# Kernel optimization log

Measured on AMD Instinct MI355X. Metric: run time of the kernel, lower is better.

## Reference

```python
import jax, jax.numpy as jnp
import numpy as np
import math

N_HEADS = 16
DIM = 1024
D_HEAD = DIM // N_HEADS
BS, QLEN = 2, 2048


def setup_inputs() -> dict:
    key = jax.random.key(0)
    ks = jax.random.split(key, 10)
    s = 0.02
    return {
        "input": jax.random.normal(ks[0], (BS, QLEN, DIM), dtype=jnp.float32),
        "mask": jnp.ones((BS, QLEN), dtype=jnp.int32),
        "q_w": jax.random.normal(ks[1], (DIM, DIM), dtype=jnp.float32) * s,
        "q_b": jax.random.normal(ks[2], (DIM,), dtype=jnp.float32) * s,
        "k_w": jax.random.normal(ks[3], (DIM, DIM), dtype=jnp.float32) * s,
        "k_b": jax.random.normal(ks[4], (DIM,), dtype=jnp.float32) * s,
        "v_w": jax.random.normal(ks[5], (DIM, DIM), dtype=jnp.float32) * s,
        "v_b": jax.random.normal(ks[6], (DIM,), dtype=jnp.float32) * s,
        "o_w": jax.random.normal(ks[7], (DIM, DIM), dtype=jnp.float32) * s,
        "o_b": jax.random.normal(ks[8], (DIM,), dtype=jnp.float32) * s,
    }


def _shape(x, bs):
    # (bs, len, dim) -> (bs, heads, len, d_head)
    return x.reshape(bs, -1, N_HEADS, D_HEAD).transpose(0, 2, 1, 3)


def reference(input, mask, q_w, q_b, k_w, k_b, v_w, v_b, o_w, o_b):
    bs, qlen, dim = input.shape
    # projections (torch Linear: x @ W^T + b)
    q = _shape(input @ q_w.T + q_b, bs)
    k = _shape(input @ k_w.T + k_b, bs)
    v = _shape(input @ v_w.T + v_b, bs)
    q = q / math.sqrt(D_HEAD)
    # scores: (bs, heads, qlen, klen)
    scores = jnp.einsum("bhqd,bhkd->bhqk", q, k)
    pad = (mask == 0)[:, None, None, :]  # (bs,1,1,klen)
    scores = jnp.where(pad, -jnp.inf, scores)
    weights = jax.nn.softmax(scores.astype(jnp.float32), axis=-1).astype(scores.dtype)
    # dropout p=0.0 (eval) -> identity
    context = jnp.einsum("bhqk,bhkd->bhqd", weights, v)
    context = context.transpose(0, 2, 1, 3).reshape(bs, qlen, dim)
    return context @ o_w.T + o_b
```

## Files before the change

kernel.cpp:

```cpp
#include <hip/hip_runtime.h>


#define BS    2
#define QLEN  2048
#define DIM   1024
#define NH    16
#define DH    64
#define MTOK  (BS * QLEN)

#define QSCALE 0.18033688011112042f

typedef __attribute__((ext_vector_type(8))) short short8;
typedef __attribute__((ext_vector_type(4))) float float4_t;
typedef __attribute__((ext_vector_type(4))) int   int4_t;

__device__ __forceinline__ ushort f2bf(float f) {
    unsigned u = __float_as_uint(f);
    return (ushort)((u + 0x7fffu + ((u >> 16) & 1u)) >> 16);
}
__device__ __forceinline__ short8 pack8(float4 a0, float4 a1) {
    short8 r;
    r[0] = (short)f2bf(a0.x); r[1] = (short)f2bf(a0.y);
    r[2] = (short)f2bf(a0.z); r[3] = (short)f2bf(a0.w);
    r[4] = (short)f2bf(a1.x); r[5] = (short)f2bf(a1.y);
    r[6] = (short)f2bf(a1.z); r[7] = (short)f2bf(a1.w);
    return r;
}

__device__ __forceinline__ void glds16(const void* g, void* l) {
    __builtin_amdgcn_global_load_lds(
        (const __attribute__((address_space(1))) unsigned int*)g,
        (__attribute__((address_space(3))) unsigned int*)l, 16, 0, 0);
}

__global__ __launch_bounds__(256) void conv_all(
    const float* __restrict__ x,  const float* __restrict__ qw,
    const float* __restrict__ kw, const float* __restrict__ vw,
    const float* __restrict__ ow,
    ushort* __restrict__ Xbf, ushort* __restrict__ Wbf)
{
    const int blk = blockIdx.x;
    const float* s; ushort* d; size_t base;
    if (blk < 4096)      { s = x;  d = Xbf;             base = (size_t)blk * 1024; }
    else if (blk < 5120) { s = qw; d = Wbf;             base = (size_t)(blk - 4096) * 1024; }
    else if (blk < 6144) { s = kw; d = Wbf + 1048576;   base = (size_t)(blk - 5120) * 1024; }
    else if (blk < 7168) { s = vw; d = Wbf + 2097152;   base = (size_t)(blk - 6144) * 1024; }
    else                 { s = ow; d = Wbf + 3145728;   base = (size_t)(blk - 7168) * 1024; }
    const size_t i = base + threadIdx.x * 4;
    float4 v = *(const float4*)(s + i);
    ushort4 o;
    o.x = f2bf(v.x); o.y = f2bf(v.y); o.z = f2bf(v.z); o.w = f2bf(v.w);
    *(ushort4*)(d + i) = o;
}

__global__ __launch_bounds__(256) void transpose_v(
    const ushort* __restrict__ Vrow, ushort* __restrict__ Vt)
{
    __shared__ ushort T[64][72];
    const int tid  = threadIdx.x;
    const int tile = blockIdx.x;
    const int bh   = blockIdx.y;
    const int b = bh >> 4, h = bh & 15;

    #pragma unroll
    for (int rep = 0; rep < 2; ++rep) {
        int ch = tid + rep * 256;
        int tok = ch >> 3, seg = ch & 7;
        uint4 v = *(const uint4*)(Vrow + (size_t)(b * QLEN + tile * 64 + tok) * DIM
                                        + h * DH + seg * 8);
        *(uint4*)&T[tok][seg * 8] = v;
    }
    __syncthreads();
    #pragma unroll
    for (int rep = 0; rep < 2; ++rep) {
        int ch = tid + rep * 256;
        int dim = ch >> 3, tseg = ch & 7;
        ushort t0 = T[tseg * 8 + 0][dim], t1 = T[tseg * 8 + 1][dim];
        ushort t2 = T[tseg * 8 + 2][dim], t3 = T[tseg * 8 + 3][dim];
        ushort t4 = T[tseg * 8 + 4][dim], t5 = T[tseg * 8 + 5][dim];
        ushort t6 = T[tseg * 8 + 6][dim], t7 = T[tseg * 8 + 7][dim];
        uint4 o;
        o.x = (unsigned)t0 | ((unsigned)t1 << 16);
        o.y = (unsigned)t2 | ((unsigned)t3 << 16);
        o.z = (unsigned)t4 | ((unsigned)t5 << 16);
        o.w = (unsigned)t6 | ((unsigned)t7 << 16);
        *(uint4*)(Vt + (size_t)bh * DH * QLEN + (size_t)dim * QLEN
                      + tile * 64 + tseg * 8) = o;
    }
}

__global__ __launch_bounds__(256) void gemm_qkv(
    const ushort* __restrict__ A, const ushort* __restrict__ Bw,
    const float* __restrict__ bias0, const float* __restrict__ bias1,
    const float* __restrict__ bias2,
    ushort* __restrict__ outQ, ushort* __restrict__ outK, ushort* __restrict__ outVt)
{
    __shared__ ushort As[128 * 64];
    __shared__ ushort Bs[128 * 64];
    const int tid  = threadIdx.x;
    const int w    = tid >> 6;
    const int lane = tid & 63;
    const int r15  = lane & 15;
    const int quad = lane >> 4;
    const int nblk = 3072 >> 7;
    const int brow = blockIdx.x / nblk;
    const int bcol = blockIdx.x - brow * nblk;
    const int wrow = (w >> 1) * 64;
    const int wcol = (w & 1) * 64;
    const int K = DIM;

    float4_t acc[4][4];
    #pragma unroll
    for (int i = 0; i < 4; ++i)
        #pragma unroll
        for (int j = 0; j < 4; ++j)
            acc[i][j] = (float4_t){0.f, 0.f, 0.f, 0.f};

    int chS[4];
    const ushort* gaS[4];
    const ushort* gbS[4];
    #pragma unroll
    for (int rep = 0; rep < 4; ++rep) {
        const int ch  = w * 256 + rep * 64 + lane;
        const int row = ch >> 3;
        const int g   = (ch & 7) ^ (row & 7);
        chS[rep] = ch;
        gaS[rep] = A  + (size_t)(brow * 128 + row) * K + g * 8;
        gbS[rep] = Bw + (size_t)(bcol * 128 + row) * K + g * 8;
    }
    const int xg = r15 & 7;

    for (int k0 = 0; k0 < K; k0 += 64) {
        __syncthreads();
        #pragma unroll
        for (int rep = 0; rep < 4; ++rep) {
            glds16(gaS[rep] + k0, As + chS[rep] * 8);
            glds16(gbS[rep] + k0, Bs + chS[rep] * 8);
        }
        __syncthreads();

        #pragma unroll
        for (int hh = 0; hh < 2; ++hh) {
            const int ph = ((hh * 4 + quad) ^ xg) * 8;
            short8 af[4], bf[4];
            #pragma unroll
            for (int ms = 0; ms < 4; ++ms)
                af[ms] = *(const short8*)&As[(wrow + ms * 16 + r15) * 64 + ph];
            #pragma unroll
            for (int ns = 0; ns < 4; ++ns)
                bf[ns] = *(const short8*)&Bs[(wcol + ns * 16 + r15) * 64 + ph];
            #pragma unroll
            for (int ms = 0; ms < 4; ++ms)
                #pragma unroll
                for (int ns = 0; ns < 4; ++ns)
                    acc[ms][ns] = __builtin_amdgcn_mfma_f32_16x16x32_bf16(
                        af[ms], bf[ns], acc[ms][ns], 0, 0, 0);
        }
    }

    #pragma unroll
    for (int ms = 0; ms < 4; ++ms) {
        const int rowg = brow * 128 + wrow + ms * 16 + quad * 4;
        #pragma unroll
        for (int ns = 0; ns < 4; ++ns) {
            const int colg = bcol * 128 + wcol + ns * 16 + r15;
            if (colg < 1024) {
                const float bb = bias0[colg];
                #pragma unroll
                for (int r = 0; r < 4; ++r)
                    outQ[(size_t)(rowg + r) * 1024 + colg] =
                        f2bf((acc[ms][ns][r] + bb) * QSCALE);
            } else if (colg < 2048) {
                const float bb = bias1[colg - 1024];
                #pragma unroll
                for (int r = 0; r < 4; ++r)
                    outK[(size_t)(rowg + r) * 1024 + (colg - 1024)] =
                        f2bf(acc[ms][ns][r] + bb);
            } else {
                const int vcol = colg - 2048;
                const int hh = vcol >> 6, dd = vcol & 63;
                const float bb = bias2[vcol];
                const int bidx = rowg >> 11;
                const int tloc = rowg & 2047;
                ushort4 o4;
                o4.x = f2bf(acc[ms][ns][0] + bb);
                o4.y = f2bf(acc[ms][ns][1] + bb);
                o4.z = f2bf(acc[ms][ns][2] + bb);
                o4.w = f2bf(acc[ms][ns][3] + bb);
                *(ushort4*)&outVt[((size_t)(bidx * 16 + hh) * 64 + dd) * QLEN + tloc] = o4;
            }
        }
    }
}

__global__ __launch_bounds__(256) void gemm_o(
    const ushort* __restrict__ A, const ushort* __restrict__ Bw,
    const float* __restrict__ bias, float* __restrict__ Out)
{
    __shared__ ushort As[128 * 64];
    __shared__ ushort Bs[64 * 64];
    const int tid  = threadIdx.x;
    const int w    = tid >> 6;
    const int lane = tid & 63;
    const int r15  = lane & 15;
    const int quad = lane >> 4;
    const int brow = blockIdx.x >> 4;
    const int bcol = blockIdx.x & 15;
    const int wrow = w * 32;
    const int K = DIM;

    float4_t acc[2][4];
    #pragma unroll
    for (int i = 0; i < 2; ++i)
        #pragma unroll
        for (int j = 0; j < 4; ++j)
            acc[i][j] = (float4_t){0.f, 0.f, 0.f, 0.f};

    int chA[4];  const ushort* gaS[4];
    #pragma unroll
    for (int rep = 0; rep < 4; ++rep) {
        const int ch  = w * 256 + rep * 64 + lane;
        const int row = ch >> 3;
        const int g   = (ch & 7) ^ (row & 7);
        chA[rep] = ch;
        gaS[rep] = A + (size_t)(brow * 128 + row) * K + g * 8;
    }
    int chB[2];  const ushort* gbS[2];
    #pragma unroll
    for (int rep = 0; rep < 2; ++rep) {
        const int ch  = w * 128 + rep * 64 + lane;
        const int row = ch >> 3;
        const int g   = (ch & 7) ^ (row & 7);
        chB[rep] = ch;
        gbS[rep] = Bw + (size_t)(bcol * 64 + row) * K + g * 8;
    }
    const int xg = r15 & 7;

    for (int k0 = 0; k0 < K; k0 += 64) {
        __syncthreads();
        #pragma unroll
        for (int rep = 0; rep < 4; ++rep)
            glds16(gaS[rep] + k0, As + chA[rep] * 8);
        #pragma unroll
        for (int rep = 0; rep < 2; ++rep)
            glds16(gbS[rep] + k0, Bs + chB[rep] * 8);
        __syncthreads();

        #pragma unroll
        for (int hh = 0; hh < 2; ++hh) {
            const int ph = ((hh * 4 + quad) ^ xg) * 8;
            short8 af[2], bf[4];
            #pragma unroll
            for (int ms = 0; ms < 2; ++ms)
                af[ms] = *(const short8*)&As[(wrow + ms * 16 + r15) * 64 + ph];
            #pragma unroll
            for (int ns = 0; ns < 4; ++ns)
                bf[ns] = *(const short8*)&Bs[(ns * 16 + r15) * 64 + ph];
            #pragma unroll
            for (int ms = 0; ms < 2; ++ms)
                #pragma unroll
                for (int ns = 0; ns < 4; ++ns)
                    acc[ms][ns] = __builtin_amdgcn_mfma_f32_16x16x32_bf16(
                        af[ms], bf[ns], acc[ms][ns], 0, 0, 0);
        }
    }

    #pragma unroll
    for (int ms = 0; ms < 2; ++ms) {
        const int rowg = brow * 128 + wrow + ms * 16 + quad * 4;
        #pragma unroll
        for (int ns = 0; ns < 4; ++ns) {
            const int colg = bcol * 64 + ns * 16 + r15;
            const float bb = bias[colg];
            #pragma unroll
            for (int r = 0; r < 4; ++r)
                Out[(size_t)(rowg + r) * 1024 + colg] = acc[ms][ns][r] + bb;
        }
    }
}

__global__ __launch_bounds__(256) void gemm_f32in_bf16out(
    const float* __restrict__ X, const float* __restrict__ W,
    const float* __restrict__ B, ushort* __restrict__ Out,
    int M, int N, int K, float scale)
{
    const int lane = threadIdx.x & 63;
    const int wid  = (blockIdx.x * blockDim.x + threadIdx.x) >> 6;
    const int tilesN = N >> 4;
    const int tm = wid / tilesN;
    const int tn = wid - tm * tilesN;
    const int r15  = lane & 15;
    const int quad = lane >> 4;

    const float* xp = X + (size_t)(tm * 16 + r15) * K + quad * 8;
    const float* wp = W + (size_t)(tn * 16 + r15) * K + quad * 8;

    float4_t acc = {0.f, 0.f, 0.f, 0.f};
    for (int k0 = 0; k0 < K; k0 += 32) {
        float4 a0 = *(const float4*)(xp + k0);
        float4 a1 = *(const float4*)(xp + k0 + 4);
        float4 b0 = *(const float4*)(wp + k0);
        float4 b1 = *(const float4*)(wp + k0 + 4);
        acc = __builtin_amdgcn_mfma_f32_16x16x32_bf16(pack8(a0, a1), pack8(b0, b1), acc, 0, 0, 0);
    }
    const int col  = tn * 16 + r15;
    const float bias = B[col];
    const int row0 = tm * 16 + quad * 4;
    #pragma unroll
    for (int r = 0; r < 4; ++r)
        Out[(size_t)(row0 + r) * N + col] = f2bf((acc[r] + bias) * scale);
}

__global__ __launch_bounds__(256) void gemm_bf16in_f32out(
    const ushort* __restrict__ X, const float* __restrict__ W,
    const float* __restrict__ B, float* __restrict__ Out,
    int M, int N, int K)
{
    const int lane = threadIdx.x & 63;
    const int wid  = (blockIdx.x * blockDim.x + threadIdx.x) >> 6;
    const int tilesN = N >> 4;
    const int tm = wid / tilesN;
    const int tn = wid - tm * tilesN;
    const int r15  = lane & 15;
    const int quad = lane >> 4;

    const ushort* xp = X + (size_t)(tm * 16 + r15) * K + quad * 8;
    const float*  wp = W + (size_t)(tn * 16 + r15) * K + quad * 8;

    float4_t acc = {0.f, 0.f, 0.f, 0.f};
    for (int k0 = 0; k0 < K; k0 += 32) {
        short8 a = *(const short8*)(xp + k0);
        float4 b0 = *(const float4*)(wp + k0);
        float4 b1 = *(const float4*)(wp + k0 + 4);
        acc = __builtin_amdgcn_mfma_f32_16x16x32_bf16(a, pack8(b0, b1), acc, 0, 0, 0);
    }
    const int col  = tn * 16 + r15;
    const float bias = B[col];
    const int row0 = tm * 16 + quad * 4;
    #pragma unroll
    for (int r = 0; r < 4; ++r)
        Out[(size_t)(row0 + r) * N + col] = acc[r] + bias;
}

__global__ __launch_bounds__(256, 2) void flash_attn(
    const ushort* __restrict__ Qb, const ushort* __restrict__ Kb,
    const ushort* __restrict__ Vt, const int* __restrict__ mask,
    ushort* __restrict__ Cb)
{
    __shared__ __align__(16) ushort Ks[2][64][64];
    __shared__ __align__(16) ushort Vs[4][64][64];
    __shared__ __align__(16) float  Mb[QLEN];

    const int tid  = threadIdx.x;
    const int w    = tid >> 6;
    const int lane = tid & 63;
    const int r15  = lane & 15;
    const int quad = lane >> 4;
    const int bh = blockIdx.y;
    const int b = bh >> 4, h = bh & 15;

    {
        const int4* m4 = (const int4*)(mask + b * QLEN);
        #pragma unroll
        for (int rep = 0; rep < 2; ++rep) {
            const int idx = tid + rep * 256;
            int4 mv = m4[idx];
            float4 o;
            o.x = mv.x ? 0.f : -INFINITY;
            o.y = mv.y ? 0.f : -INFINITY;
            o.z = mv.z ? 0.f : -INFINITY;
            o.w = mv.w ? 0.f : -INFINITY;
            *(float4*)&Mb[idx * 4] = o;
        }
    }

    const int qbase = blockIdx.x * 128 + w * 32;
    const ushort* qp = Qb + (size_t)(b * QLEN + qbase + r15) * DIM + h * DH + quad * 8;
    short8 qf[2][2];
    qf[0][0] = *(const short8*)(qp);
    qf[0][1] = *(const short8*)(qp + 32);
    qf[1][0] = *(const short8*)(qp + 16 * DIM);
    qf[1][1] = *(const short8*)(qp + 16 * DIM + 32);

    const ushort* kg = Kb + (size_t)b * QLEN * DIM + h * DH;
    const ushort* vg = Vt + (size_t)bh * DH * QLEN;

    const int a0 = tid >> 3, seg = tid & 7;
    const int krow0 = (((a0 & 7) >> 2) << 4) + (((a0 >> 3) & 3) << 2) + (a0 & 3);
    const int sK = (seg ^ (krow0 & 7)) << 3;
    const int sV = (seg ^ (a0 & 7)) << 3;
    const int xq = (quad ^ (r15 & 7)) << 3;

    float4_t o[2][4];
    float4_t ol[2];
    #pragma unroll
    for (int rg = 0; rg < 2; ++rg) {
        ol[rg] = (float4_t){0.f, 0.f, 0.f, 0.f};
        #pragma unroll
        for (int ds = 0; ds < 4; ++ds)
            o[rg][ds] = (float4_t){0.f, 0.f, 0.f, 0.f};
    }
    short8 ones8;
    #pragma unroll
    for (int i = 0; i < 8; ++i) ones8[i] = (short)0x3F80;

    uint4 kr0, kr1, vr0, vr1;
    int pkA[4][2][2], pkB[4][2][2];

#define LOAD_TILE(KT) do {                                                    \
    kr0 = *(const uint4*)(kg + (size_t)((KT) + a0     ) * DIM  + seg * 8);    \
    kr1 = *(const uint4*)(kg + (size_t)((KT) + a0 + 32) * DIM  + seg * 8);    \
    vr0 = *(const uint4*)(vg + (size_t)(a0     ) * QLEN + (KT) + seg * 8);    \
    vr1 = *(const uint4*)(vg + (size_t)(a0 + 32) * QLEN + (KT) + seg * 8);    \
} while (0)

#define STORE_TILE(KBUF, VBUF) do {                                           \
    *(uint4*)&Ks[KBUF][krow0     ][sK] = kr0;                                 \
    *(uint4*)&Ks[KBUF][krow0 + 32][sK] = kr1;                                 \
    *(uint4*)&Vs[VBUF][a0        ][sV] = vr0;                                 \
    *(uint4*)&Vs[VBUF][a0 + 32   ][sV] = vr1;                                 \
} while (0)

#define S_PHASE(KBUF, KT, PK) do {                                            \
    _Pragma("unroll")                                                         \
    for (int ks = 0; ks < 4; ++ks) {                                          \
        const ushort* krow = &Ks[KBUF][ks * 16 + r15][0];                     \
        short8 kf0 = *(const short8*)(krow + xq);                             \
        short8 kf1 = *(const short8*)(krow + (xq ^ 32));                      \
        const float4 mb = *(const float4*)&Mb[(KT) + ((ks >> 1) << 5)         \
                                              + (quad << 3) + ((ks & 1) << 2)]; \
        _Pragma("unroll")                                                     \
        for (int rg = 0; rg < 2; ++rg) {                                      \
            float4_t s = {0.f, 0.f, 0.f, 0.f};                                \
            s = __builtin_amdgcn_mfma_f32_16x16x32_bf16(kf0, qf[rg][0], s, 0, 0, 0); \
            s = __builtin_amdgcn_mfma_f32_16x16x32_bf16(kf1, qf[rg][1], s, 0, 0, 0); \
            unsigned u0 = __float_as_uint(__builtin_amdgcn_exp2f(s[0] + mb.x)); \
            unsigned u1 = __float_as_uint(__builtin_amdgcn_exp2f(s[1] + mb.y)); \
            unsigned u2 = __float_as_uint(__builtin_amdgcn_exp2f(s[2] + mb.z)); \
            unsigned u3 = __float_as_uint(__builtin_amdgcn_exp2f(s[3] + mb.w)); \
            PK[ks][rg][0] = __builtin_amdgcn_perm(u1, u0, 0x07060302);        \
            PK[ks][rg][1] = __builtin_amdgcn_perm(u3, u2, 0x07060302);        \
        }                                                                     \
    }                                                                         \
} while (0)

#define PV_PHASE(VBUF, PK) do {                                               \
    _Pragma("unroll")                                                         \
    for (int ck = 0; ck < 2; ++ck) {                                          \
        short8 vf[4];                                                         \
        _Pragma("unroll")                                                     \
        for (int ds = 0; ds < 4; ++ds)                                        \
            vf[ds] = *(const short8*)(&Vs[VBUF][ds * 16 + r15][0] + (xq ^ (ck << 5))); \
        _Pragma("unroll")                                                     \
        for (int rg = 0; rg < 2; ++rg) {                                      \
            int4_t pfi = { PK[2 * ck][rg][0], PK[2 * ck][rg][1],              \
                           PK[2 * ck + 1][rg][0], PK[2 * ck + 1][rg][1] };    \
            short8 pf = __builtin_bit_cast(short8, pfi);                      \
            _Pragma("unroll")                                                 \
            for (int ds = 0; ds < 4; ++ds)                                    \
                o[rg][ds] = __builtin_amdgcn_mfma_f32_16x16x32_bf16(          \
                    pf, vf[ds], o[rg][ds], 0, 0, 0);                          \
            ol[rg] = __builtin_amdgcn_mfma_f32_16x16x32_bf16(                 \
                pf, ones8, ol[rg], 0, 0, 0);                                  \
        }                                                                     \
    }                                                                         \
} while (0)

    LOAD_TILE(0);
    STORE_TILE(0, 0);
    LOAD_TILE(64);
    __syncthreads();
    S_PHASE(0, 0, pkA);
    STORE_TILE(1, 1);
    __syncthreads();
    LOAD_TILE(128);

    for (int kb = 0; kb < 1792; kb += 256) {
        S_PHASE(1, kb + 64, pkB);  PV_PHASE(0, pkA);
        STORE_TILE(0, 2); __syncthreads(); LOAD_TILE(kb + 192);
        S_PHASE(0, kb + 128, pkA); PV_PHASE(1, pkB);
        STORE_TILE(1, 3); __syncthreads(); LOAD_TILE(kb + 256);
        S_PHASE(1, kb + 192, pkB); PV_PHASE(2, pkA);
        STORE_TILE(0, 0); __syncthreads(); LOAD_TILE(kb + 320);
        S_PHASE(0, kb + 256, pkA); PV_PHASE(3, pkB);
        STORE_TILE(1, 1); __syncthreads(); LOAD_TILE(kb + 384);
    }

    S_PHASE(1, 1856, pkB); PV_PHASE(0, pkA);
    STORE_TILE(0, 2); __syncthreads(); LOAD_TILE(1984);
    S_PHASE(0, 1920, pkA); PV_PHASE(1, pkB);
    STORE_TILE(1, 3); __syncthreads();
    S_PHASE(1, 1984, pkB); PV_PHASE(2, pkA);
    PV_PHASE(3, pkB);

#undef LOAD_TILE
#undef STORE_TILE
#undef S_PHASE
#undef PV_PHASE

    #pragma unroll
    for (int rg = 0; rg < 2; ++rg) {
        #pragma unroll
        for (int r = 0; r < 4; ++r) {
            const float ir = 1.f / fmaxf(ol[rg][r], 1e-30f);
            const size_t rb = (size_t)(b * QLEN + qbase + rg * 16 + quad * 4 + r) * DIM
                              + h * DH;
            Cb[rb +  0 + r15] = f2bf(o[rg][0][r] * ir);
            Cb[rb + 16 + r15] = f2bf(o[rg][1][r] * ir);
            Cb[rb + 32 + r15] = f2bf(o[rg][2][r] * ir);
            Cb[rb + 48 + r15] = f2bf(o[rg][3][r] * ir);
        }
    }
}

extern "C" void kernel_launch(void* const* d_in, const int* in_sizes, int n_in,
                              void* d_out, int out_size, void* d_ws, size_t ws_size,
                              hipStream_t stream)
{
    const float* x    = (const float*)d_in[0];
    const int*   mask = (const int*)d_in[1];
    const float* q_w  = (const float*)d_in[2];
    const float* q_b  = (const float*)d_in[3];
    const float* k_w  = (const float*)d_in[4];
    const float* k_b  = (const float*)d_in[5];
    const float* v_w  = (const float*)d_in[6];
    const float* v_b  = (const float*)d_in[7];
    const float* o_w  = (const float*)d_in[8];
    const float* o_b  = (const float*)d_in[9];
    float* out = (float*)d_out;

    const size_t SEG = (size_t)MTOK * DIM;
    ushort* Qbf = (ushort*)d_out;
    ushort* Xbf = Qbf + SEG;
    ushort* Kb  = (ushort*)d_ws;
    ushort* Cb  = Kb + SEG;
    ushort* Vt  = Cb + SEG;
    ushort* Wbf = Vt + SEG;

    const bool big = ws_size >= (size_t)32 * 1024 * 1024;

    if (big) {
        conv_all<<<8192, 256, 0, stream>>>(x, q_w, k_w, v_w, o_w, Xbf, Wbf);
        gemm_qkv<<<(MTOK / 128) * (3072 / 128), 256, 0, stream>>>(
            Xbf, Wbf, q_b, k_b, v_b, Qbf, Kb, Vt);
        flash_attn<<<dim3(QLEN / 128, BS * NH), 256, 0, stream>>>(Qbf, Kb, Vt, mask, Cb);
        gemm_o<<<(MTOK / 128) * (DIM / 64), 256, 0, stream>>>(
            Cb, Wbf + 3 * (size_t)(DIM * DIM), o_b, out);
    } else {
        const int tiles   = (MTOK / 16) * (DIM / 16);
        const int gblocks = tiles / 4;
        gemm_f32in_bf16out<<<gblocks, 256, 0, stream>>>(x, q_w, q_b, Qbf, MTOK, DIM, DIM, QSCALE);
        gemm_f32in_bf16out<<<gblocks, 256, 0, stream>>>(x, k_w, k_b, Kb,  MTOK, DIM, DIM, 1.0f);
        gemm_f32in_bf16out<<<gblocks, 256, 0, stream>>>(x, v_w, v_b, Cb,  MTOK, DIM, DIM, 1.0f);
        transpose_v<<<dim3(QLEN / 64, BS * NH), 256, 0, stream>>>(Cb, Vt);
        flash_attn<<<dim3(QLEN / 128, BS * NH), 256, 0, stream>>>(Qbf, Kb, Vt, mask, Cb);
        gemm_bf16in_f32out<<<tiles / 4, 256, 0, stream>>>(Cb, o_w, o_b, out, MTOK, DIM, DIM);
    }
}
```

Baseline: 194.8 us.

## Double-buffer LDS tiles in QKV and output GEMMs with XCD-aware block remap

Both bf16 GEMMs now use two LDS buffers, so the global-to-LDS copy of the next K slice is issued before the MFMAs on the current slice, with one barrier per iteration instead of two. The QKV GEMM halves its K-step to 32 with a matching 4-way swizzle to keep LDS use unchanged. Block indices are also remapped so that blocks landing on the same XCD cover a compact tile region, which should improve L2 reuse. The risks are more barriers in the QKV kernel from the shorter K-step, and whether the hardcoded remap exactly matches the grid size.

```diff
diff --git a/kernel.cpp b/kernel.cpp
--- a/kernel.cpp
+++ b/kernel.cpp
@@ -95,16 +95,17 @@
     const float* __restrict__ bias2,
     ushort* __restrict__ outQ, ushort* __restrict__ outK, ushort* __restrict__ outVt)
 {
-    __shared__ ushort As[128 * 64];
-    __shared__ ushort Bs[128 * 64];
+    __shared__ ushort As[2][128 * 32];
+    __shared__ ushort Bs[2][128 * 32];
     const int tid  = threadIdx.x;
     const int w    = tid >> 6;
     const int lane = tid & 63;
     const int r15  = lane & 15;
     const int quad = lane >> 4;
-    const int nblk = 3072 >> 7;
-    const int brow = blockIdx.x / nblk;
-    const int bcol = blockIdx.x - brow * nblk;
+    const int xcd = blockIdx.x & 7;
+    const int lid = blockIdx.x >> 3;
+    const int brow = (xcd & 3) * 8  + (lid & 7);
+    const int bcol = (xcd >> 2) * 12 + (lid >> 3);
     const int wrow = (w >> 1) * 64;
     const int wcol = (w & 1) * 64;
     const int K = DIM;
@@ -116,46 +117,51 @@
         for (int j = 0; j < 4; ++j)
             acc[i][j] = (float4_t){0.f, 0.f, 0.f, 0.f};
 
-    int chS[4];
-    const ushort* gaS[4];
-    const ushort* gbS[4];
-    #pragma unroll
-    for (int rep = 0; rep < 4; ++rep) {
-        const int ch  = w * 256 + rep * 64 + lane;
-        const int row = ch >> 3;
-        const int g   = (ch & 7) ^ (row & 7);
+    int chS[2];
+    const ushort* gaS[2];
+    const ushort* gbS[2];
+    #pragma unroll
+    for (int rep = 0; rep < 2; ++rep) {
+        const int ch  = w * 128 + rep * 64 + lane;
+        const int row = ch >> 2;
+        const int g   = (ch & 3) ^ ((row >> 1) & 3);
         chS[rep] = ch;
         gaS[rep] = A  + (size_t)(brow * 128 + row) * K + g * 8;
         gbS[rep] = Bw + (size_t)(bcol * 128 + row) * K + g * 8;
     }
-    const int xg = r15 & 7;
-
-    for (int k0 = 0; k0 < K; k0 += 64) {
+    const int ph = (quad ^ ((r15 >> 1) & 3)) * 8;
+
+    #pragma unroll
+    for (int rep = 0; rep < 2; ++rep) {
+        glds16(gaS[rep], &As[0][chS[rep] * 8]);
+        glds16(gbS[rep], &Bs[0][chS[rep] * 8]);
+    }
+    __syncthreads();
+
+    int p = 0;
+    for (int k0 = 0; k0 < K; k0 += 32) {
+        if (k0 + 32 < K) {
+            #pragma unroll
+            for (int rep = 0; rep < 2; ++rep) {
+                glds16(gaS[rep] + k0 + 32, &As[p ^ 1][chS[rep] * 8]);
+                glds16(gbS[rep] + k0 + 32, &Bs[p ^ 1][chS[rep] * 8]);
+            }
+        }
+        short8 af[4], bf[4];
+        #pragma unroll
+        for (int ms = 0; ms < 4; ++ms)
+            af[ms] = *(const short8*)&As[p][(wrow + ms * 16 + r15) * 32 + ph];
+        #pragma unroll
+        for (int ns = 0; ns < 4; ++ns)
+            bf[ns] = *(const short8*)&Bs[p][(wcol + ns * 16 + r15) * 32 + ph];
+        #pragma unroll
+        for (int ms = 0; ms < 4; ++ms)
+            #pragma unroll
+            for (int ns = 0; ns < 4; ++ns)
+                acc[ms][ns] = __builtin_amdgcn_mfma_f32_16x16x32_bf16(
+                    af[ms], bf[ns], acc[ms][ns], 0, 0, 0);
         __syncthreads();
-        #pragma unroll
-        for (int rep = 0; rep < 4; ++rep) {
-            glds16(gaS[rep] + k0, As + chS[rep] * 8);
-            glds16(gbS[rep] + k0, Bs + chS[rep] * 8);
-        }
-        __syncthreads();
-
-        #pragma unroll
-        for (int hh = 0; hh < 2; ++hh) {
-            const int ph = ((hh * 4 + quad) ^ xg) * 8;
-            short8 af[4], bf[4];
-            #pragma unroll
-            for (int ms = 0; ms < 4; ++ms)
-                af[ms] = *(const short8*)&As[(wrow + ms * 16 + r15) * 64 + ph];
-            #pragma unroll
-            for (int ns = 0; ns < 4; ++ns)
-                bf[ns] = *(const short8*)&Bs[(wcol + ns * 16 + r15) * 64 + ph];
-            #pragma unroll
-            for (int ms = 0; ms < 4; ++ms)
-                #pragma unroll
-                for (int ns = 0; ns < 4; ++ns)
-                    acc[ms][ns] = __builtin_amdgcn_mfma_f32_16x16x32_bf16(
-                        af[ms], bf[ns], acc[ms][ns], 0, 0, 0);
-        }
+        p ^= 1;
     }
 
     #pragma unroll
@@ -197,15 +203,17 @@
     const ushort* __restrict__ A, const ushort* __restrict__ Bw,
     const float* __restrict__ bias, float* __restrict__ Out)
 {
-    __shared__ ushort As[128 * 64];
-    __shared__ ushort Bs[64 * 64];
+    __shared__ ushort As[2][128 * 64];
+    __shared__ ushort Bs[2][64 * 64];
     const int tid  = threadIdx.x;
     const int w    = tid >> 6;
     const int lane = tid & 63;
     const int r15  = lane & 15;
     const int quad = lane >> 4;
-    const int brow = blockIdx.x >> 4;
-    const int bcol = blockIdx.x & 15;
+    const int xcd = blockIdx.x & 7;
+    const int lid = blockIdx.x >> 3;
+    const int brow = (xcd & 3) * 8 + (lid & 7);
+    const int bcol = (xcd >> 2) * 8 + (lid >> 3);
     const int wrow = w * 32;
     const int K = DIM;
 
@@ -236,26 +244,34 @@
     }
     const int xg = r15 & 7;
 
+    #pragma unroll
+    for (int rep = 0; rep < 4; ++rep)
+        glds16(gaS[rep], &As[0][chA[rep] * 8]);
+    #pragma unroll
+    for (int rep = 0; rep < 2; ++rep)
+        glds16(gbS[rep], &Bs[0][chB[rep] * 8]);
+    __syncthreads();
+
+    int p = 0;
     for (int k0 = 0; k0 < K; k0 += 64) {
-        __syncthreads();
-        #pragma unroll
-        for (int rep = 0; rep < 4; ++rep)
-            glds16(gaS[rep] + k0, As + chA[rep] * 8);
-        #pragma unroll
-        for (int rep = 0; rep < 2; ++rep)
-            glds16(gbS[rep] + k0, Bs + chB[rep] * 8);
-        __syncthreads();
-
+        if (k0 + 64 < K) {
+            #pragma unroll
+            for (int rep = 0; rep < 4; ++rep)
+                glds16(gaS[rep] + k0 + 64, &As[p ^ 1][chA[rep] * 8]);
+            #pragma unroll
+            for (int rep = 0; rep < 2; ++rep)
+                glds16(gbS[rep] + k0 + 64, &Bs[p ^ 1][chB[rep] * 8]);
+        }
         #pragma unroll
         for (int hh = 0; hh < 2; ++hh) {
             const int ph = ((hh * 4 + quad) ^ xg) * 8;
             short8 af[2], bf[4];
             #pragma unroll
             for (int ms = 0; ms < 2; ++ms)
-                af[ms] = *(const short8*)&As[(wrow + ms * 16 + r15) * 64 + ph];
+                af[ms] = *(const short8*)&As[p][(wrow + ms * 16 + r15) * 64 + ph];
             #pragma unroll
             for (int ns = 0; ns < 4; ++ns)
-                bf[ns] = *(const short8*)&Bs[(ns * 16 + r15) * 64 + ph];
+                bf[ns] = *(const short8*)&Bs[p][(ns * 16 + r15) * 64 + ph];
             #pragma unroll
             for (int ms = 0; ms < 2; ++ms)
                 #pragma unroll
@@ -263,6 +279,8 @@
                     acc[ms][ns] = __builtin_amdgcn_mfma_f32_16x16x32_bf16(
                         af[ms], bf[ns], acc[ms][ns], 0, 0, 0);
         }
+        __syncthreads();
+        p ^= 1;
     }
 
     #pragma unroll
```

Measured after the change: 191.5 us. Within noise of the previous version (-1.7%).
